# Kernel tuning notes

Hardware: AMD Instinct MI355X
Metric: run time of the kernel (lower is better)

## Reference

```python
import jax, jax.numpy as jnp
import numpy as np

NUM_CAPSULE = 5
DIM_CAPSULE = 5
ROUTINGS = 4
T_EPSILON = 1e-07


def squash(x, axis=-1):
    # Note: this module's 'squash' is pure norm-normalization (no v^2/(1+v^2) factor)
    s_squared_norm = jnp.sum(x * x, axis=axis, keepdims=True)
    return x / jnp.sqrt(s_squared_norm + T_EPSILON)


def setup_inputs() -> dict:
    key = jax.random.key(0)
    k1, k2 = jax.random.split(key)
    batch, seq, d_in = 1024, 512, 120
    x = jax.random.normal(k1, (batch, seq, d_in), dtype=jnp.float32)
    # xavier_normal for fan_in=120, fan_out=25
    std = float(np.sqrt(2.0 / (d_in + NUM_CAPSULE * DIM_CAPSULE)))
    W = jax.random.normal(k2, (1, d_in, NUM_CAPSULE * DIM_CAPSULE), dtype=jnp.float32) * std
    return {"x": x, "W": W}


def reference(x, W):
    batch, inp, _ = x.shape
    # u_hat_vecs: [batch, num_capsule, input_num_capsule, dim_capsule]
    u_hat = jnp.matmul(x, W[0])  # [b, inp, 25]
    u_hat = u_hat.reshape(batch, inp, NUM_CAPSULE, DIM_CAPSULE).transpose(0, 2, 1, 3)
    b = jnp.zeros((batch, NUM_CAPSULE, inp), dtype=u_hat.dtype)
    outputs = None
    for i in range(ROUTINGS):
        # torch code softmaxes over the num_capsule axis (dim 1 of b)
        c = jax.nn.softmax(b, axis=1)  # [b, ncaps, inp]
        outputs = squash(jnp.einsum('bij,bijk->bik', c, u_hat))  # [b, ncaps, dcap]
        if i < ROUTINGS - 1:
            b = jnp.einsum('bik,bijk->bij', outputs, u_hat)
    return outputs
```

## Files before the change

kernel.cpp:

```cpp
#include <hip/hip_runtime.h>


#define NCAP 5
#define DCAP 5
#define NOUT 25
#define DIN 120
#define SEQ 512
#define ROUTINGS 4
#define NQ   30

__global__ __launch_bounds__(512) void caps_kernel(
    const float* __restrict__ x,
    const float* __restrict__ W,
    float* __restrict__ out)
{
    const int b    = blockIdx.x;
    const int t    = threadIdx.x;
    const int lane = t & 63;
    const int wv   = t >> 6;

    __shared__ float red[8][NOUT];

    const float* xr = x + (size_t)b * SEQ * DIN + (size_t)t * DIN;

    float4 rv[NQ];
#pragma unroll
    for (int q = 0; q < NQ; ++q)
        rv[q] = *(const float4*)(xr + 4 * q);

    float acc[NOUT];
#pragma unroll
    for (int j = 0; j < NOUT; ++j) acc[j] = 0.f;

#pragma unroll
    for (int q = 0; q < NQ; ++q) {
        const float* wr = W + (4 * q) * NOUT;
#pragma unroll
        for (int j = 0; j < NOUT; ++j) {
            float w0 = wr[j];
            float w1 = wr[j + NOUT];
            float w2 = wr[j + 2 * NOUT];
            float w3 = wr[j + 3 * NOUT];
            acc[j] = fmaf(rv[q].w, w3,
                     fmaf(rv[q].z, w2,
                     fmaf(rv[q].y, w1,
                     fmaf(rv[q].x, w0, acc[j]))));
        }
    }

    float bb[NCAP];
#pragma unroll
    for (int c = 0; c < NCAP; ++c) bb[c] = 0.f;

    float o[NOUT];

    for (int it = 0; it < ROUTINGS; ++it) {
        float m = bb[0];
#pragma unroll
        for (int c = 1; c < NCAP; ++c) m = fmaxf(m, bb[c]);
        float e[NCAP]; float se = 0.f;
#pragma unroll
        for (int c = 0; c < NCAP; ++c) { e[c] = __expf(bb[c] - m); se += e[c]; }
        float inv = 1.f / se;

        float p[NOUT];
#pragma unroll
        for (int c = 0; c < NCAP; ++c) {
            float cc = e[c] * inv;
#pragma unroll
            for (int k = 0; k < DCAP; ++k)
                p[c*DCAP + k] = cc * acc[c*DCAP + k];
        }

#pragma unroll
        for (int d = 1; d < 64; d <<= 1)
#pragma unroll
            for (int j = 0; j < NOUT; ++j) p[j] += __shfl_xor(p[j], d, 64);

        if (lane == 0) {
#pragma unroll
            for (int j = 0; j < NOUT; ++j) red[wv][j] = p[j];
        }
        __syncthreads();
        float s[NOUT];
#pragma unroll
        for (int j = 0; j < NOUT; ++j)
            s[j] = red[0][j] + red[1][j] + red[2][j] + red[3][j]
                 + red[4][j] + red[5][j] + red[6][j] + red[7][j];
        __syncthreads();

#pragma unroll
        for (int c = 0; c < NCAP; ++c) {
            float ss = 0.f;
#pragma unroll
            for (int k = 0; k < DCAP; ++k)
                ss = fmaf(s[c*DCAP + k], s[c*DCAP + k], ss);
            float sc = rsqrtf(ss + 1e-7f);
#pragma unroll
            for (int k = 0; k < DCAP; ++k) o[c*DCAP + k] = s[c*DCAP + k] * sc;
        }

        if (it < ROUTINGS - 1) {
#pragma unroll
            for (int c = 0; c < NCAP; ++c) {
                float d0 = 0.f;
#pragma unroll
                for (int k = 0; k < DCAP; ++k)
                    d0 = fmaf(o[c*DCAP + k], acc[c*DCAP + k], d0);
                bb[c] = d0;
            }
        }
    }

    if (t < NOUT) out[(size_t)b * NOUT + t] = o[t];
}

extern "C" void kernel_launch(void* const* d_in, const int* in_sizes, int n_in,
                              void* d_out, int out_size, void* d_ws, size_t ws_size,
                              hipStream_t stream) {
    const float* x   = (const float*)d_in[0];
    const float* W   = (const float*)d_in[1];
    float*       o   = (float*)d_out;
    const int batch  = in_sizes[0] / (SEQ * DIN);
    caps_kernel<<<dim3(batch), dim3(512), 0, stream>>>(x, W, o);
}
```

Baseline: 486.3 us.

## Split fused kernel into separate projection GEMM and routing kernels via workspace

Splits the single fused kernel in two. The first kernel computes u_hat per row, loading x in 6 chunks of 20 floats instead of holding all 120 in registers, and writes it to workspace in a transposed [batch][25][seq] layout. The second kernel does routing with 256 threads per batch element, each handling two rows, which halves the cross-wave reduction. This is meant to cut register pressure and raise occupancy in the memory-bound projection, at the cost of an extra round trip of about 52 MB of u_hat through global memory and a second launch.

```diff
diff --git a/kernel.cpp b/kernel.cpp
--- a/kernel.cpp
+++ b/kernel.cpp
@@ -7,11 +7,51 @@
 #define DIN 120
 #define SEQ 512
 #define ROUTINGS 4
-#define NQ   30
 
-__global__ __launch_bounds__(512) void caps_kernel(
+__global__ __launch_bounds__(256) void gemm_kernel(
     const float* __restrict__ x,
     const float* __restrict__ W,
+    float* __restrict__ uh)
+{
+    const int gid = blockIdx.x * 256 + threadIdx.x;
+    const int b   = gid >> 9;
+    const int r   = gid & 511;
+    const float* xr = x + (size_t)gid * DIN;
+
+    float acc[NOUT];
+#pragma unroll
+    for (int j = 0; j < NOUT; ++j) acc[j] = 0.f;
+
+#pragma unroll 1
+    for (int ch = 0; ch < 6; ++ch) {
+        float4 v[5];
+#pragma unroll
+        for (int u = 0; u < 5; ++u)
+            v[u] = *(const float4*)(xr + ch * 20 + 4 * u);
+#pragma unroll
+        for (int u = 0; u < 5; ++u) {
+            const float* wr = W + (ch * 20 + 4 * u) * NOUT;
+#pragma unroll
+            for (int j = 0; j < NOUT; ++j) {
+                float w0 = wr[j];
+                float w1 = wr[j + NOUT];
+                float w2 = wr[j + 2 * NOUT];
+                float w3 = wr[j + 3 * NOUT];
+                acc[j] = fmaf(v[u].w, w3,
+                         fmaf(v[u].z, w2,
+                         fmaf(v[u].y, w1,
+                         fmaf(v[u].x, w0, acc[j]))));
+            }
+        }
+    }
+
+    float* ub = uh + (size_t)b * NOUT * SEQ + r;
+#pragma unroll
+    for (int j = 0; j < NOUT; ++j) ub[(size_t)j * SEQ] = acc[j];
+}
+
+__global__ __launch_bounds__(256) void route_kernel(
+    const float* __restrict__ uh,
     float* __restrict__ out)
 {
     const int b    = blockIdx.x;
@@ -19,57 +59,41 @@
     const int lane = t & 63;
     const int wv   = t >> 6;
 
-    __shared__ float red[8][NOUT];
+    __shared__ float red[4][NOUT];
 
-    const float* xr = x + (size_t)b * SEQ * DIN + (size_t)t * DIN;
-
-    float4 rv[NQ];
+    const float* ub = uh + (size_t)b * NOUT * SEQ;
+    float u0[NOUT], u1[NOUT];
 #pragma unroll
-    for (int q = 0; q < NQ; ++q)
-        rv[q] = *(const float4*)(xr + 4 * q);
-
-    float acc[NOUT];
-#pragma unroll
-    for (int j = 0; j < NOUT; ++j) acc[j] = 0.f;
-
-#pragma unroll
-    for (int q = 0; q < NQ; ++q) {
-        const float* wr = W + (4 * q) * NOUT;
-#pragma unroll
-        for (int j = 0; j < NOUT; ++j) {
-            float w0 = wr[j];
-            float w1 = wr[j + NOUT];
-            float w2 = wr[j + 2 * NOUT];
-            float w3 = wr[j + 3 * NOUT];
-            acc[j] = fmaf(rv[q].w, w3,
-                     fmaf(rv[q].z, w2,
-                     fmaf(rv[q].y, w1,
-                     fmaf(rv[q].x, w0, acc[j]))));
-        }
+    for (int j = 0; j < NOUT; ++j) {
+        u0[j] = ub[(size_t)j * SEQ + t];
+        u1[j] = ub[(size_t)j * SEQ + t + 256];
     }
 
-    float bb[NCAP];
+    float bb0[NCAP], bb1[NCAP];
 #pragma unroll
-    for (int c = 0; c < NCAP; ++c) bb[c] = 0.f;
+    for (int c = 0; c < NCAP; ++c) { bb0[c] = 0.f; bb1[c] = 0.f; }
 
-    float o[NOUT];
+    float s[NOUT], sc[NCAP];
 
     for (int it = 0; it < ROUTINGS; ++it) {
-        float m = bb[0];
+        float m0 = bb0[0], m1 = bb1[0];
 #pragma unroll
-        for (int c = 1; c < NCAP; ++c) m = fmaxf(m, bb[c]);
-        float e[NCAP]; float se = 0.f;
+        for (int c = 1; c < NCAP; ++c) { m0 = fmaxf(m0, bb0[c]); m1 = fmaxf(m1, bb1[c]); }
+        float e0[NCAP], e1[NCAP]; float se0 = 0.f, se1 = 0.f;
 #pragma unroll
-        for (int c = 0; c < NCAP; ++c) { e[c] = __expf(bb[c] - m); se += e[c]; }
-        float inv = 1.f / se;
+        for (int c = 0; c < NCAP; ++c) {
+            e0[c] = __expf(bb0[c] - m0); se0 += e0[c];
+            e1[c] = __expf(bb1[c] - m1); se1 += e1[c];
+        }
+        float i0 = 1.f / se0, i1 = 1.f / se1;
 
         float p[NOUT];
 #pragma unroll
         for (int c = 0; c < NCAP; ++c) {
-            float cc = e[c] * inv;
+            float c0 = e0[c] * i0, c1 = e1[c] * i1;
 #pragma unroll
             for (int k = 0; k < DCAP; ++k)
-                p[c*DCAP + k] = cc * acc[c*DCAP + k];
+                p[c*DCAP + k] = fmaf(c0, u0[c*DCAP + k], c1 * u1[c*DCAP + k]);
         }
 
 #pragma unroll
@@ -82,11 +106,9 @@
             for (int j = 0; j < NOUT; ++j) red[wv][j] = p[j];
         }
         __syncthreads();
-        float s[NOUT];
 #pragma unroll
         for (int j = 0; j < NOUT; ++j)
-            s[j] = red[0][j] + red[1][j] + red[2][j] + red[3][j]
-                 + red[4][j] + red[5][j] + red[6][j] + red[7][j];
+            s[j] = red[0][j] + red[1][j] + red[2][j] + red[3][j];
         __syncthreads();
 
 #pragma unroll
@@ -95,24 +117,25 @@
 #pragma unroll
             for (int k = 0; k < DCAP; ++k)
                 ss = fmaf(s[c*DCAP + k], s[c*DCAP + k], ss);
-            float sc = rsqrtf(ss + 1e-7f);
-#pragma unroll
-            for (int k = 0; k < DCAP; ++k) o[c*DCAP + k] = s[c*DCAP + k] * sc;
+            sc[c] = rsqrtf(ss + 1e-7f);
         }
 
         if (it < ROUTINGS - 1) {
 #pragma unroll
             for (int c = 0; c < NCAP; ++c) {
-                float d0 = 0.f;
+                float d0 = 0.f, d1 = 0.f;
 #pragma unroll
-                for (int k = 0; k < DCAP; ++k)
-                    d0 = fmaf(o[c*DCAP + k], acc[c*DCAP + k], d0);
-                bb[c] = d0;
+                for (int k = 0; k < DCAP; ++k) {
+                    float oc = s[c*DCAP + k] * sc[c];
+                    d0 = fmaf(oc, u0[c*DCAP + k], d0);
+                    d1 = fmaf(oc, u1[c*DCAP + k], d1);
+                }
+                bb0[c] = d0; bb1[c] = d1;
             }
         }
     }
 
-    if (t < NOUT) out[(size_t)b * NOUT + t] = o[t];
+    if (t < NOUT) out[(size_t)b * NOUT + t] = s[t] * sc[t / DCAP];
 }
 
 extern "C" void kernel_launch(void* const* d_in, const int* in_sizes, int n_in,
@@ -121,6 +144,9 @@
     const float* x   = (const float*)d_in[0];
     const float* W   = (const float*)d_in[1];
     float*       o   = (float*)d_out;
+    float*       uh  = (float*)d_ws;
     const int batch  = in_sizes[0] / (SEQ * DIN);
-    caps_kernel<<<dim3(batch), dim3(512), 0, stream>>>(x, W, o);
+
+    gemm_kernel<<<dim3(batch * 2), dim3(256), 0, stream>>>(x, W, uh);
+    route_kernel<<<dim3(batch),    dim3(256), 0, stream>>>(uh, o);
 }
```

After: 465.6 us. 1.04x faster.
